# Kernel tuning notes

Measured on AMD Instinct MI355X. Metric: run time of the kernel, lower is better.

The kernel has to match this reference:

```python
import jax, jax.numpy as jnp
from jax import lax
import numpy as np

# Straight-through-estimator sign (standard BNN binarization):
# fwd: sign(x) with sign(0)=+1; bwd: pass gradient where |x|<=1 (hardtanh STE).
@jax.custom_vjp
def sign_ste(x):
    return jnp.where(x >= 0, 1.0, -1.0).astype(x.dtype)

def _sign_fwd(x):
    return sign_ste(x), x

def _sign_bwd(x, g):
    return (g * (jnp.abs(x) <= 1.0).astype(g.dtype),)

sign_ste.defvjp(_sign_fwd, _sign_bwd)

EPS = 1e-5  # BatchNorm eps (torch default)

def bn4(x, g, b):  # BatchNorm2d, training-mode batch stats, x: [N,C,H,W]
    m = x.mean((0, 2, 3), keepdims=True)
    v = x.var((0, 2, 3), keepdims=True)
    return g[None, :, None, None] * (x - m) * lax.rsqrt(v + EPS) + b[None, :, None, None]

def bn1(x, g, b):  # BatchNorm1d, x: [N,C]
    m = x.mean(0, keepdims=True)
    v = x.var(0, keepdims=True)
    return g * (x - m) * lax.rsqrt(v + EPS) + b

def bconv(x, W, b, first):
    # BinarizedConv2d: binarize weights always; binarize input except first layer.
    xb = x if first else sign_ste(x)
    y = lax.conv_general_dilated(xb, sign_ste(W), (1, 1), [(1, 1), (1, 1)],
                                 dimension_numbers=('NCHW', 'OIHW', 'NCHW'))
    return y + b[None, :, None, None]

def maxpool2(x):
    return lax.reduce_window(x, -jnp.inf, lax.max, (1, 1, 2, 2), (1, 1, 2, 2), 'VALID')

def ht(x):  # Hardtanh
    return jnp.clip(x, -1.0, 1.0)

CONV_CH = [(3, 64), (64, 128), (128, 256), (256, 256), (256, 512), (512, 512), (512, 512), (512, 512)]
LIN_CH = [(512, 512), (512, 512), (512, 10)]
POOL_AFTER = (0, 1, 3, 5, 7)  # conv indices followed by MaxPool2d

def setup_inputs():
    key = jax.random.key(0)
    ks = iter(jax.random.split(key, 64))
    d = {"x": jax.random.normal(next(ks), (256, 3, 32, 32), jnp.float32)}
    for i, (ci, co) in enumerate(CONV_CH):
        d[f"cw{i}"] = jax.random.normal(next(ks), (co, ci, 3, 3), jnp.float32) * 0.1
        d[f"cb{i}"] = jnp.zeros((co,), jnp.float32)
        d[f"cg{i}"] = jnp.ones((co,), jnp.float32)
        d[f"ct{i}"] = jnp.zeros((co,), jnp.float32)
    for i, (ci, co) in enumerate(LIN_CH):
        d[f"lw{i}"] = jax.random.normal(next(ks), (co, ci), jnp.float32) * 0.1
        d[f"lb{i}"] = jnp.zeros((co,), jnp.float32)
        d[f"lg{i}"] = jnp.ones((co,), jnp.float32)
        d[f"lt{i}"] = jnp.zeros((co,), jnp.float32)
    return d

def _forward(x, cw, cb, cg, ct, lw, lb, lg, lt):
    h = x
    for i in range(8):
        h = bconv(h, cw[i], cb[i], i == 0)
        if i in POOL_AFTER:
            h = maxpool2(h)
        h = ht(bn4(h, cg[i], ct[i]))
    h = h.reshape(h.shape[0], -1)  # [N, 512] after 5 pools on 32x32
    for i in range(3):
        h = sign_ste(h) @ sign_ste(lw[i]).T + lb[i]  # BinarizedLinear
        h = bn1(h, lg[i], lt[i])
        if i < 2:
            h = ht(h)  # Dropout is identity in eval mode
    return jax.nn.log_softmax(h, axis=-1)

def reference(x,
              cw0, cb0, cg0, ct0, cw1, cb1, cg1, ct1, cw2, cb2, cg2, ct2,
              cw3, cb3, cg3, ct3, cw4, cb4, cg4, ct4, cw5, cb5, cg5, ct5,
              cw6, cb6, cg6, ct6, cw7, cb7, cg7, ct7,
              lw0, lb0, lg0, lt0, lw1, lb1, lg1, lt1, lw2, lb2, lg2, lt2):
    cw = [cw0, cw1, cw2, cw3, cw4, cw5, cw6, cw7]
    cb = [cb0, cb1, cb2, cb3, cb4, cb5, cb6, cb7]
    cg = [cg0, cg1, cg2, cg3, cg4, cg5, cg6, cg7]
    ct = [ct0, ct1, ct2, ct3, ct4, ct5, ct6, ct7]
    lw = [lw0, lw1, lw2]
    lb = [lb0, lb1, lb2]
    lg = [lg0, lg1, lg2]
    lt = [lt0, lt1, lt2]
    return _forward(x, cw, cb, cg, ct, lw, lb, lg, lt)
```

## Files before the change

kernel.cpp:

```cpp
#include <hip/hip_runtime.h>
#include <hip/hip_bf16.h>

typedef unsigned long long u64;

#define EPSV 1e-5

__device__ __forceinline__ int imax(int a, int b) { return a > b ? a : b; }
__device__ __forceinline__ int iclamp(int v, int lo, int hi) { return v < lo ? lo : (v > hi ? hi : v); }

struct PrepArgs {
    const float* src[10];
    u64* dst[10];
    int CW[10];
    int Co[10];
    int taps[10];
    int rowbase[11];
    u64* accs;
    int naccs;
};

__global__ __launch_bounds__(256) void prep_kernel(PrepArgs a) {
    __shared__ float buf[4608];
    const int blk = blockIdx.x;
    int z = blk * 19 + threadIdx.x;
    if (threadIdx.x < 19 && z < a.naccs) a.accs[z] = 0ULL;

    int l = 0;
    while (l < 9 && blk >= a.rowbase[l + 1]) ++l;
    const int row = blk - a.rowbase[l];
    const int CW = a.CW[l];
    const int taps = a.taps[l];
    const int nf = CW * 64 * taps;
    const float* srow = a.src[l] + (size_t)row * nf;
    for (int i = threadIdx.x; i < nf; i += 256) buf[i] = srow[i];
    __syncthreads();
    const int t = threadIdx.x;
    if (t < taps * CW) {
        u64 bits = 0;
        if (taps == 9) {
            int k = t % 9, w = t / 9;
            for (int j = 0; j < 64; ++j) bits |= (u64)(buf[(w * 64 + j) * 9 + k] >= 0.f) << j;
            a.dst[l][(size_t)(k * CW + w) * a.Co[l] + row] = bits;
        } else {
            for (int j = 0; j < 64; ++j) bits |= (u64)(buf[t * 64 + j] >= 0.f) << j;
            a.dst[l][(size_t)row * CW + t] = bits;
        }
    }
}

__global__ __launch_bounds__(256) void conv0_lane(const float* __restrict__ x,
                                                  const float* __restrict__ wgt,
                                                  float* __restrict__ out,
                                                  double* __restrict__ dacc) {
    const int lane = threadIdx.x & 63;
    const int wave = threadIdx.x >> 6;
    float ws[27];
#pragma unroll
    for (int j = 0; j < 27; ++j) ws[j] = (wgt[lane * 27 + j] >= 0.f) ? 1.f : -1.f;

    const int gp0 = blockIdx.x * 32;
    const int n = gp0 >> 8;
    const int ypA = (gp0 >> 4) & 15;
    const int yb = 2 * ypA - 1;

    __shared__ float simg[3][6][34];
    const float* xb = x + (size_t)n * 3072;
    for (int t = threadIdx.x; t < 612; t += 256) {
        int ci = t / 204;
        int rem = t % 204;
        int r = rem / 34;
        int cc = rem % 34;
        int yy = yb + r;
        int xx = cc - 1;
        float v = 0.f;
        if ((unsigned)yy < 32u && (unsigned)xx < 32u) v = xb[(ci * 32 + yy) * 32 + xx];
        simg[ci][r][cc] = v;
    }
    __syncthreads();

    double s1 = 0.0, s2 = 0.0;
#pragma unroll 2
    for (int pi = 0; pi < 8; ++pi) {
        const int lp = wave * 8 + pi;
        const int gp = gp0 + lp;
        const int xp = lp & 15;
        const int rbase = 2 * (lp >> 4);
        const int cbase = 2 * xp;
        float win[3][4][4];
#pragma unroll
        for (int ci = 0; ci < 3; ++ci)
#pragma unroll
            for (int r = 0; r < 4; ++r)
#pragma unroll
                for (int c = 0; c < 4; ++c) win[ci][r][c] = simg[ci][rbase + r][cbase + c];
        float a00 = 0.f, a01 = 0.f, a10 = 0.f, a11 = 0.f;
#pragma unroll
        for (int ci = 0; ci < 3; ++ci)
#pragma unroll
            for (int ky = 0; ky < 3; ++ky)
#pragma unroll
                for (int kx = 0; kx < 3; ++kx) {
                    float wv = ws[ci * 9 + ky * 3 + kx];
                    a00 += win[ci][ky][kx] * wv;
                    a01 += win[ci][ky][kx + 1] * wv;
                    a10 += win[ci][ky + 1][kx] * wv;
                    a11 += win[ci][ky + 1][kx + 1] * wv;
                }
        float val = fmaxf(fmaxf(a00, a01), fmaxf(a10, a11));
        out[(size_t)gp * 64 + lane] = val;
        s1 += (double)val;
        s2 += (double)val * (double)val;
    }
    __shared__ double sh1[4][64], sh2[4][64];
    sh1[wave][lane] = s1;
    sh2[wave][lane] = s2;
    __syncthreads();
    if (threadIdx.x < 64) {
        double t1 = 0.0, t2 = 0.0;
#pragma unroll
        for (int r = 0; r < 4; ++r) { t1 += sh1[r][threadIdx.x]; t2 += sh2[r][threadIdx.x]; }
        double* sh = dacc + (size_t)(blockIdx.x & 7) * 1024;
        atomicAdd(&sh[2 * threadIdx.x], t1);
        atomicAdd(&sh[2 * threadIdx.x + 1], t2);
    }
}

__global__ __launch_bounds__(256) void bnpack_i(const short* __restrict__ in,
                                                const u64* __restrict__ iacc,
                                                const float* __restrict__ g,
                                                const float* __restrict__ b,
                                                u64* __restrict__ act, int Co, int wshift,
                                                int count) {
    __shared__ int2 sthr[520];
    for (int i = threadIdx.x; i < Co; i += 256) {
        long long S1 = 0, S2 = 0;
#pragma unroll
        for (int s = 0; s < 8; ++s) {
            S1 += (long long)iacc[s * 1024 + 2 * i];
            S2 += (long long)iacc[s * 1024 + 2 * i + 1];
        }
        double m = (double)S1 / count;
        double var = (double)S2 / count - m * m;
        double sc = (double)g[i] / sqrt(var + EPSV);
        int2 r;
        if (sc == 0.0) r = make_int2(b[i] >= 0.f ? (int)0x80000000 : 0x7fffffff, 0);
        else {
            double t = m - (double)b[i] / sc;
            if (t > 1.0e9) t = 1.0e9;
            if (t < -1.0e9) t = -1.0e9;
            r = (sc > 0.0) ? make_int2((int)ceil(t), 0) : make_int2((int)floor(t), 1);
        }
        sthr[(i >> 6) * 65 + (i & 63)] = r;
    }
    __syncthreads();
    int tid = blockIdx.x * 256 + threadIdx.x;
    int part = tid & 3;
    int word = tid >> 2;
    int w = word & ((1 << wshift) - 1);
    int pix = word >> wshift;
    const int4* r4 = (const int4*)(in + (size_t)pix * Co + (w << 6) + part * 16);
    u64 bits = 0;
#pragma unroll
    for (int q = 0; q < 2; ++q) {
        int4 v = r4[q];
        int words4[4] = {v.x, v.y, v.z, v.w};
#pragma unroll
        for (int u = 0; u < 4; ++u) {
#pragma unroll
            for (int h = 0; h < 2; ++h) {
                int c = part * 16 + q * 8 + u * 2 + h;
                int val = (int)(short)((h == 0) ? (words4[u] & 0xffff) : ((unsigned)words4[u] >> 16));
                int2 t = sthr[w * 65 + c];
                bool bit = t.y ? (val <= t.x) : (val >= t.x);
                bits |= (u64)bit << c;
            }
        }
    }
    bits |= __shfl_xor(bits, 1);
    bits |= __shfl_xor(bits, 2);
    if (part == 0) act[word] = bits;
}

template <int CW, int HIN, bool POOL, int WC, bool INTERIOR>
__device__ __forceinline__ void row_accum(const u64* __restrict__ inb,
                                          const u64* __restrict__ wpkT, int Co, int co,
                                          const int* yoff, const bool* ry, int* cnt) {
    constexpr int HP = POOL ? HIN / 2 : HIN;
    constexpr int WS = POOL ? 4 : 3;
    constexpr int NA = POOL ? 4 : 1;
#pragma unroll 1
    for (int w0 = 0; w0 < CW; w0 += WC) {
        u64 wg[9 * WC];
#pragma unroll
        for (int k = 0; k < 9; ++k)
#pragma unroll
            for (int w = 0; w < WC; ++w)
                wg[k * WC + w] = wpkT[(size_t)(k * CW + w0 + w) * Co + co];
        u64 cur[WS][WS][WC];
#pragma unroll
        for (int d = 0; d < WS; ++d) {
            int cc = d - 1;
            int ccc = cc < 0 ? 0 : cc;
#pragma unroll
            for (int r = 0; r < WS; ++r) {
                const u64* p = inb + yoff[r] + ccc * CW + w0;
                if (WC == 1) {
                    cur[r][d][0] = p[0];
                } else {
                    ulonglong2 v = *(const ulonglong2*)p;
                    cur[r][d][0] = v.x;
                    cur[r][d][1] = v.y;
                }
            }
        }
#pragma unroll
        for (int xp = 0; xp < HP; ++xp) {
            if constexpr (POOL) {
#pragma unroll
                for (int py = 0; py < 2; ++py)
#pragma unroll
                    for (int qx = 0; qx < 2; ++qx)
#pragma unroll
                        for (int ky = 0; ky < 3; ++ky)
#pragma unroll
                            for (int kx = 0; kx < 3; ++kx) {
                                int d = qx + kx;
                                int cc = 2 * xp + d - 1;
                                if (cc >= 0 && cc < HIN) {
#pragma unroll
                                    for (int w = 0; w < WC; ++w) {
                                        int pc = (int)__popcll(cur[py + ky][d][w] ^
                                                               wg[(ky * 3 + kx) * WC + w]);
                                        if constexpr (INTERIOR)
                                            cnt[xp * NA + py * 2 + qx] += pc;
                                        else
                                            cnt[xp * NA + py * 2 + qx] += ry[py + ky] ? pc : 0;
                                    }
                                }
                            }
            } else {
#pragma unroll
                for (int ky = 0; ky < 3; ++ky)
#pragma unroll
                    for (int kx = 0; kx < 3; ++kx) {
                        int cc = xp + kx - 1;
                        if (cc >= 0 && cc < HIN) {
#pragma unroll
                            for (int w = 0; w < WC; ++w) {
                                int pc = (int)__popcll(cur[ky][kx][w] ^
                                                       wg[(ky * 3 + kx) * WC + w]);
                                if constexpr (INTERIOR)
                                    cnt[xp] += pc;
                                else
                                    cnt[xp] += ry[ky] ? pc : 0;
                            }
                        }
                    }
            }
            if (xp < HP - 1) {
                if constexpr (POOL) {
#pragma unroll
                    for (int r = 0; r < WS; ++r)
#pragma unroll
                        for (int w = 0; w < WC; ++w) {
                            cur[r][0][w] = cur[r][2][w];
                            cur[r][1][w] = cur[r][3][w];
                        }
#pragma unroll
                    for (int dd = 2; dd < 4; ++dd) {
                        int cc = 2 * (xp + 1) + dd - 1;
                        int ccc = cc >= HIN ? HIN - 1 : cc;
#pragma unroll
                        for (int r = 0; r < WS; ++r) {
                            const u64* p = inb + yoff[r] + ccc * CW + w0;
                            if (WC == 1) {
                                cur[r][dd][0] = p[0];
                            } else {
                                ulonglong2 v = *(const ulonglong2*)p;
                                cur[r][dd][0] = v.x;
                                cur[r][dd][1] = v.y;
                            }
                        }
                    }
                } else {
#pragma unroll
                    for (int r = 0; r < WS; ++r)
#pragma unroll
                        for (int w = 0; w < WC; ++w) {
                            cur[r][0][w] = cur[r][1][w];
                            cur[r][1][w] = cur[r][2][w];
                        }
                    int cc = xp + 2;
                    int ccc = cc >= HIN ? HIN - 1 : cc;
#pragma unroll
                    for (int r = 0; r < WS; ++r) {
                        const u64* p = inb + yoff[r] + ccc * CW + w0;
                        if (WC == 1) {
                            cur[r][2][0] = p[0];
                        } else {
                            ulonglong2 v = *(const ulonglong2*)p;
                            cur[r][2][0] = v.x;
                            cur[r][2][1] = v.y;
                        }
                    }
                }
            }
        }
    }
}

template <int CW, int HIN, bool POOL, int WC, bool FIRST>
__global__ __launch_bounds__(256) void bconv_row_f(const void* __restrict__ inprev,
                                                   const void* __restrict__ pstats,
                                                   const float* __restrict__ pg,
                                                   const float* __restrict__ pb, int pcount,
                                                   const u64* __restrict__ wpkT,
                                                   short* __restrict__ out,
                                                   u64* __restrict__ iacc, int Co) {
    constexpr int HP = POOL ? HIN / 2 : HIN;
    constexpr int WS = POOL ? 4 : 3;
    constexpr int NA = POOL ? 4 : 1;
    constexpr int ROWS = POOL ? 10 : 6;
    constexpr int Ci = CW * 64;
    __shared__ __align__(16) u64 sU[ROWS * HIN * CW];
    __shared__ int2 sthr[CW * 65];
    __shared__ float2 sthf[64];

    if constexpr (FIRST) {
        if (threadIdx.x < 64) {
            const double* dacc = (const double*)pstats;
            int i = threadIdx.x;
            double S1 = 0.0, S2 = 0.0;
#pragma unroll
            for (int s = 0; s < 8; ++s) {
                S1 += dacc[s * 1024 + 2 * i];
                S2 += dacc[s * 1024 + 2 * i + 1];
            }
            double m = S1 / pcount;
            double var = S2 / pcount - m * m;
            double sc = (double)pg[i] / sqrt(var + EPSV);
            float2 r;
            if (sc == 0.0) r = make_float2(pb[i] >= 0.f ? -3.0e38f : 3.0e38f, 1.f);
            else {
                double t = m - (double)pb[i] / sc;
                r = make_float2((float)t, sc > 0.0 ? 1.f : -1.f);
            }
            sthf[i] = r;
        }
    } else {
        const u64* pacc = (const u64*)pstats;
        for (int i = threadIdx.x; i < Ci; i += 256) {
            long long S1 = 0, S2 = 0;
#pragma unroll
            for (int s = 0; s < 8; ++s) {
                S1 += (long long)pacc[s * 1024 + 2 * i];
                S2 += (long long)pacc[s * 1024 + 2 * i + 1];
            }
            double m = (double)S1 / pcount;
            double var = (double)S2 / pcount - m * m;
            double sc = (double)pg[i] / sqrt(var + EPSV);
            int2 r;
            if (sc == 0.0) r = make_int2(pb[i] >= 0.f ? (int)0x80000000 : 0x7fffffff, 0);
            else {
                double t = m - (double)pb[i] / sc;
                if (t > 1.0e9) t = 1.0e9;
                if (t < -1.0e9) t = -1.0e9;
                r = (sc > 0.0) ? make_int2((int)ceil(t), 0) : make_int2((int)floor(t), 1);
            }
            sthr[(i >> 6) * 65 + (i & 63)] = r;
        }
    }
    __syncthreads();

    const int bi = blockIdx.x;
    constexpr int BPN = HP / 4;
    const int n = bi / BPN;
    const int yp0 = (bi % BPN) * 4;
    const int ylo = imax(0, (POOL ? 2 * yp0 : yp0) - 1);
    const int yhiU = POOL ? (2 * yp0 + 8) : (yp0 + 4);
    const int yhi = yhiU > HIN - 1 ? HIN - 1 : yhiU;
    const int nrows = yhi - ylo + 1;
    const int nw = nrows * HIN * CW;

    if constexpr (FIRST) {
        const float* src = (const float*)inprev;
        for (int t = threadIdx.x; t < nw; t += 256) {
            int x = t % HIN;
            int yr = t / HIN;
            int y = ylo + yr;
            const float4* p = (const float4*)(src + (size_t)((n * 16 + y) * 16 + x) * 64);
            u64 bits = 0;
#pragma unroll
            for (int q = 0; q < 16; ++q) {
                float4 v = p[q];
                float vv[4] = {v.x, v.y, v.z, v.w};
#pragma unroll
                for (int u = 0; u < 4; ++u) {
                    int c = q * 4 + u;
                    float2 th = sthf[c];
                    bool bit = (th.y > 0.f) ? (vv[u] >= th.x) : (vv[u] <= th.x);
                    bits |= (u64)bit << c;
                }
            }
            sU[t] = bits;
        }
    } else {
        const short* src = (const short*)inprev;
        for (int t = threadIdx.x; t < nw; t += 256) {
            int w = t % CW;
            int x = (t / CW) % HIN;
            int yr = t / (HIN * CW);
            int y = ylo + yr;
            const int4* p = (const int4*)(src + (size_t)((n * HIN + y) * HIN + x) * Ci + w * 64);
            u64 bits = 0;
#pragma unroll
            for (int q = 0; q < 8; ++q) {
                int4 v = p[q];
                int wd[4] = {v.x, v.y, v.z, v.w};
#pragma unroll
                for (int u = 0; u < 4; ++u) {
#pragma unroll
                    for (int h = 0; h < 2; ++h) {
                        int j = q * 8 + u * 2 + h;
                        int val = (int)(short)((h == 0) ? (wd[u] & 0xffff) : ((unsigned)wd[u] >> 16));
                        int2 th = sthr[w * 65 + j];
                        bool bit = th.y ? (val <= th.x) : (val >= th.x);
                        bits |= (u64)bit << j;
                    }
                }
            }
            sU[t] = bits;
        }
    }
    __syncthreads();

    const int lane = threadIdx.x & 63;
    const int wave = threadIdx.x >> 6;
    const int co = blockIdx.y * 64 + lane;
    const int yp = yp0 + wave;
    const int grow = n * HP + yp;
    const int y0 = (POOL ? 2 * yp : yp) - 1;
    int yoff[WS];
    bool ry[WS];
#pragma unroll
    for (int r = 0; r < WS; ++r) {
        int y = y0 + r;
        ry[r] = (unsigned)y < (unsigned)HIN;
        int yc = iclamp(y, 0, HIN - 1);
        yoff[r] = (yc - ylo) * (HIN * CW);
    }
    int cnt[HP * NA];
#pragma unroll
    for (int i = 0; i < HP * NA; ++i) cnt[i] = 0;

    if (yp > 0 && yp < HP - 1)
        row_accum<CW, HIN, POOL, WC, true>(sU, wpkT, Co, co, yoff, ry, cnt);
    else
        row_accum<CW, HIN, POOL, WC, false>(sU, wpkT, Co, co, yoff, ry, cnt);

    const int nr0 = (int)ry[0] + (int)ry[1] + (int)ry[2];
    const int nr1 = POOL ? ((int)ry[1] + (int)ry[2] + (int)ry[WS - 1]) : 0;

    int s1 = 0;
    long long s2 = 0;
    short* orow = out + (size_t)grow * HP * Co + co;
#pragma unroll
    for (int xp = 0; xp < HP; ++xp) {
        int ival;
        if constexpr (POOL) {
            int best = -2147483647;
#pragma unroll
            for (int py = 0; py < 2; ++py) {
                const int nrv = py ? nr1 : nr0;
#pragma unroll
                for (int qx = 0; qx < 2; ++qx) {
                    int ncols = 3;
                    if (xp == 0 && qx == 0) ncols = 2;
                    if (xp == HP - 1 && qx == 1) ncols = 2;
                    int v = 64 * CW * nrv * ncols - 2 * cnt[xp * NA + py * 2 + qx];
                    best = imax(best, v);
                }
            }
            ival = best;
        } else {
            const int ncols = (xp == 0 || xp == HIN - 1) ? 2 : 3;
            ival = 64 * CW * nr0 * ncols - 2 * cnt[xp];
        }
        orow[(size_t)xp * Co] = (short)ival;
        s1 += ival;
        s2 += (long long)ival * ival;
    }

    __shared__ u64 sacc[128];
    if (threadIdx.x < 128) sacc[threadIdx.x] = 0ULL;
    __syncthreads();
    atomicAdd(&sacc[lane], (u64)(long long)s1);
    atomicAdd(&sacc[64 + lane], (u64)s2);
    __syncthreads();
    u64* sh = iacc + (size_t)(blockIdx.x & 7) * 1024;
    if (threadIdx.x < 64)
        atomicAdd(&sh[2 * (blockIdx.y * 64 + threadIdx.x)], sacc[threadIdx.x]);
    else if (threadIdx.x < 128)
        atomicAdd(&sh[2 * (blockIdx.y * 64 + threadIdx.x - 64) + 1], sacc[threadIdx.x]);
}

template <int CW, int HIN, bool POOL>
__global__ __launch_bounds__(256) void bconv_tiny_f(const short* __restrict__ inprev,
                                                    const u64* __restrict__ pacc,
                                                    const float* __restrict__ pg,
                                                    const float* __restrict__ pb, int pcount,
                                                    const u64* __restrict__ wpkT,
                                                    short* __restrict__ out,
                                                    u64* __restrict__ iacc, int Co) {
    constexpr int NPX = HIN * HIN;
    constexpr int HP = POOL ? HIN / 2 : HIN;
    constexpr int Ci = CW * 64;
    __shared__ int2 sthr[CW * 65];
    __shared__ u64 sU[4][NPX * CW];

    for (int i = threadIdx.x; i < Ci; i += 256) {
        long long S1 = 0, S2 = 0;
#pragma unroll
        for (int s = 0; s < 8; ++s) {
            S1 += (long long)pacc[s * 1024 + 2 * i];
            S2 += (long long)pacc[s * 1024 + 2 * i + 1];
        }
        double m = (double)S1 / pcount;
        double var = (double)S2 / pcount - m * m;
        double sc = (double)pg[i] / sqrt(var + EPSV);
        int2 r;
        if (sc == 0.0) r = make_int2(pb[i] >= 0.f ? (int)0x80000000 : 0x7fffffff, 0);
        else {
            double t = m - (double)pb[i] / sc;
            if (t > 1.0e9) t = 1.0e9;
            if (t < -1.0e9) t = -1.0e9;
            r = (sc > 0.0) ? make_int2((int)ceil(t), 0) : make_int2((int)floor(t), 1);
        }
        sthr[(i >> 6) * 65 + (i & 63)] = r;
    }
    __syncthreads();

    const int nbase = blockIdx.x * 4;
    for (int t = threadIdx.x; t < 4 * NPX * CW; t += 256) {
        int img = t / (NPX * CW);
        int rem = t % (NPX * CW);
        int w = rem % CW;
        int i = rem / CW;
        const int4* p = (const int4*)(inprev + (size_t)((nbase + img) * NPX + i) * Ci + w * 64);
        u64 bits = 0;
#pragma unroll
        for (int q = 0; q < 8; ++q) {
            int4 v = p[q];
            int wd[4] = {v.x, v.y, v.z, v.w};
#pragma unroll
            for (int u = 0; u < 4; ++u) {
#pragma unroll
                for (int h = 0; h < 2; ++h) {
                    int j = q * 8 + u * 2 + h;
                    int val = (int)(short)((h == 0) ? (wd[u] & 0xffff) : ((unsigned)wd[u] >> 16));
                    int2 th = sthr[w * 65 + j];
                    bool bit = th.y ? (val <= th.x) : (val >= th.x);
                    bits |= (u64)bit << j;
                }
            }
        }
        sU[img][i * CW + w] = bits;
    }
    __syncthreads();

    const int lane = threadIdx.x & 63;
    const int co = blockIdx.y * 64 + lane;
    const int n = nbase + (threadIdx.x >> 6);
    const u64* inb = sU[threadIdx.x >> 6];
    int cnt[NPX];
#pragma unroll
    for (int i = 0; i < NPX; ++i) cnt[i] = 0;

#pragma unroll 2
    for (int w = 0; w < CW; ++w) {
        u64 win[NPX];
#pragma unroll
        for (int i = 0; i < NPX; ++i) win[i] = inb[i * CW + w];
#pragma unroll
        for (int k = 0; k < 9; ++k) {
            u64 wb = wpkT[(size_t)(k * CW + w) * Co + co];
            const int ky = k / 3, kx = k % 3;
#pragma unroll
            for (int py = 0; py < HIN; ++py)
#pragma unroll
                for (int px = 0; px < HIN; ++px) {
                    const int yy = py + ky - 1, xx = px + kx - 1;
                    if (yy >= 0 && yy < HIN && xx >= 0 && xx < HIN)
                        cnt[py * HIN + px] += (int)__popcll(win[yy * HIN + xx] ^ wb);
                }
        }
    }

    int fin[NPX];
#pragma unroll
    for (int py = 0; py < HIN; ++py)
#pragma unroll
        for (int px = 0; px < HIN; ++px) {
            const int nk = ((py == 0 || py == HIN - 1) ? 2 : 3) *
                           ((px == 0 || px == HIN - 1) ? 2 : 3);
            fin[py * HIN + px] = 64 * CW * nk - 2 * cnt[py * HIN + px];
        }

    short vals[HP * HP];
    if constexpr (POOL) {
#pragma unroll
        for (int py = 0; py < HP; ++py)
#pragma unroll
            for (int px = 0; px < HP; ++px)
                vals[py * HP + px] = (short)imax(
                    imax(fin[(2 * py) * HIN + 2 * px], fin[(2 * py) * HIN + 2 * px + 1]),
                    imax(fin[(2 * py + 1) * HIN + 2 * px], fin[(2 * py + 1) * HIN + 2 * px + 1]));
    } else {
#pragma unroll
        for (int i = 0; i < NPX; ++i) vals[i] = (short)fin[i];
    }
#pragma unroll
    for (int p = 0; p < HP * HP; ++p) out[(size_t)(n * HP * HP + p) * Co + co] = vals[p];

    long long s1 = 0, s2 = 0;
#pragma unroll
    for (int p = 0; p < HP * HP; ++p) {
        s1 += vals[p];
        s2 += (long long)vals[p] * vals[p];
    }
    __shared__ u64 sacc[128];
    if (threadIdx.x < 128) sacc[threadIdx.x] = 0ULL;
    __syncthreads();
    atomicAdd(&sacc[lane], (u64)s1);
    atomicAdd(&sacc[64 + lane], (u64)s2);
    __syncthreads();
    u64* sh = iacc + (size_t)(blockIdx.x & 7) * 1024;
    if (threadIdx.x < 64)
        atomicAdd(&sh[2 * (blockIdx.y * 64 + threadIdx.x)], sacc[threadIdx.x]);
    else if (threadIdx.x < 128)
        atomicAdd(&sh[2 * (blockIdx.y * 64 + threadIdx.x - 64) + 1], sacc[threadIdx.x]);
}

__global__ __launch_bounds__(256) void lin_kernel(const u64* __restrict__ hp,
                                                  const u64* __restrict__ wp,
                                                  const float* __restrict__ lb,
                                                  const float* __restrict__ g,
                                                  const float* __restrict__ bta,
                                                  u64* __restrict__ op) {
    int o = blockIdx.x;
    int n = threadIdx.x;
    const u64* hr = hp + n * 8;
    const u64* wr = wp + o * 8;
    int s = 0;
#pragma unroll
    for (int w = 0; w < 8; ++w) s += (int)__popcll(hr[w] ^ wr[w]);
    float val = (float)(512 - 2 * s) + lb[o];
    __shared__ double sh1[256], sh2[256];
    sh1[n] = (double)val;
    sh2[n] = (double)val * (double)val;
    __syncthreads();
    for (int st = 128; st > 0; st >>= 1) {
        if (n < st) {
            sh1[n] += sh1[n + st];
            sh2[n] += sh2[n + st];
        }
        __syncthreads();
    }
    __shared__ float sm, siv;
    if (n == 0) {
        double m = sh1[0] / 256.0;
        double var = sh2[0] / 256.0 - m * m;
        sm = (float)m;
        siv = (float)(1.0 / sqrt(var + EPSV));
    }
    __syncthreads();
    float zz = g[o] * (val - sm) * siv + bta[o];
    if (zz >= 0.f) atomicOr(&op[(size_t)n * 8 + (o >> 6)], 1ULL << (o & 63));
}

__global__ __launch_bounds__(256) void lin2_lsm(const u64* __restrict__ hp,
                                                const u64* __restrict__ wp,
                                                const float* __restrict__ lb,
                                                const float* __restrict__ g,
                                                const float* __restrict__ bta,
                                                float* __restrict__ out) {
    const int n = threadIdx.x;
    const int lane = n & 63;
    const int wave = n >> 6;
    u64 h[8];
#pragma unroll
    for (int w = 0; w < 8; ++w) h[w] = hp[n * 8 + w];
    float v[10];
#pragma unroll
    for (int o = 0; o < 10; ++o) {
        int s = 0;
#pragma unroll
        for (int w = 0; w < 8; ++w) s += (int)__popcll(h[w] ^ wp[o * 8 + w]);
        v[o] = (float)(512 - 2 * s) + lb[o];
    }
    __shared__ double w1[4][10], w2[4][10];
#pragma unroll
    for (int o = 0; o < 10; ++o) {
        double a = (double)v[o];
        double b = a * a;
#pragma unroll
        for (int off = 32; off > 0; off >>= 1) {
            a += __shfl_xor(a, off);
            b += __shfl_xor(b, off);
        }
        if (lane == 0) {
            w1[wave][o] = a;
            w2[wave][o] = b;
        }
    }
    __syncthreads();
    float z[10];
#pragma unroll
    for (int o = 0; o < 10; ++o) {
        double S1 = w1[0][o] + w1[1][o] + w1[2][o] + w1[3][o];
        double S2 = w2[0][o] + w2[1][o] + w2[2][o] + w2[3][o];
        double m = S1 / 256.0;
        double var = S2 / 256.0 - m * m;
        float sm = (float)m;
        float siv = (float)(1.0 / sqrt(var + EPSV));
        z[o] = g[o] * (v[o] - sm) * siv + bta[o];
    }
    float mx = z[0];
#pragma unroll
    for (int o = 1; o < 10; ++o) mx = fmaxf(mx, z[o]);
    float se = 0.f;
#pragma unroll
    for (int o = 0; o < 10; ++o) se += expf(z[o] - mx);
    float ls = logf(se);
#pragma unroll
    for (int o = 0; o < 10; ++o) out[n * 10 + o] = z[o] - mx - ls;
}

extern "C" void kernel_launch(void* const* d_in, const int* in_sizes, int n_in, void* d_out,
                              int out_size, void* d_ws, size_t ws_size, hipStream_t stream) {
    (void)in_sizes; (void)n_in; (void)out_size; (void)ws_size;
    const float* x = (const float*)d_in[0];
    const float *cw[8], *cb[8], *cg[8], *ct[8];
    for (int i = 0; i < 8; ++i) {
        cw[i] = (const float*)d_in[1 + 4 * i];
        cb[i] = (const float*)d_in[2 + 4 * i];
        cg[i] = (const float*)d_in[3 + 4 * i];
        ct[i] = (const float*)d_in[4 + 4 * i];
    }
    const float *lw[3], *lb[3], *lg[3], *lt[3];
    for (int i = 0; i < 3; ++i) {
        lw[i] = (const float*)d_in[33 + 4 * i];
        lb[i] = (const float*)d_in[34 + 4 * i];
        lg[i] = (const float*)d_in[35 + 4 * i];
        lt[i] = (const float*)d_in[36 + 4 * i];
    }

    static const int CIs[8] = {3, 64, 128, 256, 256, 512, 512, 512};
    static const int COs[8] = {64, 128, 256, 256, 512, 512, 512, 512};

    char* ws = (char*)d_ws;
    size_t off = 0;
    auto alloc = [&](size_t bytes) -> void* {
        void* p = ws + off;
        off += (bytes + 255) & ~(size_t)255;
        return p;
    };

    u64* accs = (u64*)alloc((size_t)8 * 8 * 1024 * 8);
    u64* fcs0 = (u64*)alloc(2048 * 8);
    u64* fcs1 = (u64*)alloc(2048 * 8);
    double* dacc0 = (double*)accs;
    auto iacc = [&](int layer) { return accs + (size_t)layer * 8192; };

    u64* wpkT[8] = {};
    for (int i = 1; i < 8; ++i) wpkT[i] = (u64*)alloc((size_t)COs[i] * 9 * (CIs[i] / 64) * 8);
    u64* wpl[3];
    int LO[3] = {512, 512, 10};
    for (int i = 0; i < 3; ++i) wpl[i] = (u64*)alloc((size_t)LO[i] * 8 * 8);
    u64* act7 = (u64*)alloc((size_t)256 * 8 * 8);
    float* out0 = (float*)alloc((size_t)65536 * 64 * 4);
    short* i16A = (short*)alloc((size_t)16384 * 256 * 2);
    short* i16B = (short*)alloc((size_t)16384 * 256 * 2);

    PrepArgs pa;
    int rb = 0;
    for (int i = 1; i < 8; ++i) {
        int e = i - 1;
        pa.src[e] = cw[i];
        pa.dst[e] = wpkT[i];
        pa.CW[e] = CIs[i] / 64;
        pa.Co[e] = COs[i];
        pa.taps[e] = 9;
        pa.rowbase[e] = rb;
        rb += COs[i];
    }
    for (int i = 0; i < 3; ++i) {
        int e = 7 + i;
        pa.src[e] = lw[i];
        pa.dst[e] = wpl[i];
        pa.CW[e] = 8;
        pa.Co[e] = LO[i];
        pa.taps[e] = 1;
        pa.rowbase[e] = rb;
        rb += LO[i];
    }
    pa.rowbase[10] = rb;
    pa.accs = accs;
    pa.naccs = 8 * 8 * 1024 + 2048 + 2048;
    prep_kernel<<<rb, 256, 0, stream>>>(pa);

    conv0_lane<<<2048, 256, 0, stream>>>(x, cw[0], out0, dacc0);

    bconv_row_f<1, 16, true, 1, true><<<dim3(512, 2), 256, 0, stream>>>(
        out0, dacc0, cg[0], ct[0], 65536, wpkT[1], i16A, iacc(1), 128);

    bconv_row_f<2, 8, false, 2, false><<<dim3(512, 4), 256, 0, stream>>>(
        i16A, iacc(1), cg[1], ct[1], 16384, wpkT[2], i16B, iacc(2), 256);

    bconv_row_f<4, 8, true, 2, false><<<dim3(256, 4), 256, 0, stream>>>(
        i16B, iacc(2), cg[2], ct[2], 16384, wpkT[3], i16A, iacc(3), 256);

    bconv_row_f<4, 4, false, 2, false><<<dim3(256, 8), 256, 0, stream>>>(
        i16A, iacc(3), cg[3], ct[3], 4096, wpkT[4], i16B, iacc(4), 512);

    bconv_tiny_f<8, 4, true><<<dim3(64, 8), 256, 0, stream>>>(
        i16B, iacc(4), cg[4], ct[4], 4096, wpkT[5], i16A, iacc(5), 512);

    bconv_tiny_f<8, 2, false><<<dim3(64, 8), 256, 0, stream>>>(
        i16A, iacc(5), cg[5], ct[5], 1024, wpkT[6], i16B, iacc(6), 512);

    bconv_tiny_f<8, 2, true><<<dim3(64, 8), 256, 0, stream>>>(
        i16B, iacc(6), cg[6], ct[6], 1024, wpkT[7], i16A, iacc(7), 512);

    bnpack_i<<<32, 256, 0, stream>>>(i16A, iacc(7), cg[7], ct[7], act7, 512, 3, 256);

    lin_kernel<<<512, 256, 0, stream>>>(act7, wpl[0], lb[0], lg[0], lt[0], fcs0);
    lin_kernel<<<512, 256, 0, stream>>>(fcs0, wpl[1], lb[1], lg[1], lt[1], fcs1);
    lin2_lsm<<<1, 256, 0, stream>>>(fcs1, wpl[2], lb[2], lg[2], lt[2], (float*)d_out);
}
```

Baseline: 405.9 us.

## Merge weight prep into conv0 launch and restructure linear head kernels

Weight binarization blocks are folded into the conv0 kernel as extra blocks sharing one launch, and the accumulator zeroing moves to a memset. The linear layers now write float outputs that separate pack kernels turn into bits, replacing the atomicOr packing and the single-block final layer with separate linear and log-softmax kernels. Vector 128-bit loads in the conv inner loop become scalar loads, and BN threshold code is factored into a helper. The net launch count goes up in the head, and the scalar loads may cost memory throughput.

```diff
diff --git a/kernel.cpp b/kernel.cpp
--- a/kernel.cpp
+++ b/kernel.cpp
@@ -7,6 +7,21 @@
 
 __device__ __forceinline__ int imax(int a, int b) { return a > b ? a : b; }
 __device__ __forceinline__ int iclamp(int v, int lo, int hi) { return v < lo ? lo : (v > hi ? hi : v); }
+
+__device__ __forceinline__ int2 thr_int(long long S1, long long S2, float gv, float bv, int count) {
+    double m = (double)S1 / count;
+    double var = (double)S2 / count - m * m;
+    double sc = (double)gv / sqrt(var + EPSV);
+    int2 r;
+    if (sc == 0.0) r = make_int2(bv >= 0.f ? (int)0x80000000 : 0x7fffffff, 0);
+    else {
+        double t = m - (double)bv / sc;
+        if (t > 1.0e9) t = 1.0e9;
+        if (t < -1.0e9) t = -1.0e9;
+        r = (sc > 0.0) ? make_int2((int)ceil(t), 0) : make_int2((int)floor(t), 1);
+    }
+    return r;
+}
 
 struct PrepArgs {
     const float* src[10];
@@ -15,43 +30,40 @@
     int Co[10];
     int taps[10];
     int rowbase[11];
-    u64* accs;
-    int naccs;
 };
 
-__global__ __launch_bounds__(256) void prep_kernel(PrepArgs a) {
-    __shared__ float buf[4608];
-    const int blk = blockIdx.x;
-    int z = blk * 19 + threadIdx.x;
-    if (threadIdx.x < 19 && z < a.naccs) a.accs[z] = 0ULL;
-
-    int l = 0;
-    while (l < 9 && blk >= a.rowbase[l + 1]) ++l;
-    const int row = blk - a.rowbase[l];
-    const int CW = a.CW[l];
-    const int taps = a.taps[l];
-    const int nf = CW * 64 * taps;
-    const float* srow = a.src[l] + (size_t)row * nf;
-    for (int i = threadIdx.x; i < nf; i += 256) buf[i] = srow[i];
-    __syncthreads();
-    const int t = threadIdx.x;
-    if (t < taps * CW) {
-        u64 bits = 0;
-        if (taps == 9) {
-            int k = t % 9, w = t / 9;
-            for (int j = 0; j < 64; ++j) bits |= (u64)(buf[(w * 64 + j) * 9 + k] >= 0.f) << j;
-            a.dst[l][(size_t)(k * CW + w) * a.Co[l] + row] = bits;
-        } else {
-            for (int j = 0; j < 64; ++j) bits |= (u64)(buf[t * 64 + j] >= 0.f) << j;
-            a.dst[l][(size_t)row * CW + t] = bits;
-        }
-    }
-}
-
-__global__ __launch_bounds__(256) void conv0_lane(const float* __restrict__ x,
+__global__ __launch_bounds__(256) void prep_conv0(PrepArgs a, const float* __restrict__ x,
                                                   const float* __restrict__ wgt,
                                                   float* __restrict__ out,
                                                   double* __restrict__ dacc) {
+    __shared__ __align__(16) char smem[18432];
+    if (blockIdx.x >= 2048) {
+        float* buf = (float*)smem;
+        const int blk = blockIdx.x - 2048;
+        int l = 0;
+        while (l < 9 && blk >= a.rowbase[l + 1]) ++l;
+        const int row = blk - a.rowbase[l];
+        const int CW = a.CW[l];
+        const int taps = a.taps[l];
+        const int nf = CW * 64 * taps;
+        const float* srow = a.src[l] + (size_t)row * nf;
+        for (int i = threadIdx.x; i < nf; i += 256) buf[i] = srow[i];
+        __syncthreads();
+        const int t = threadIdx.x;
+        if (t < taps * CW) {
+            u64 bits = 0;
+            if (taps == 9) {
+                int k = t % 9, w = t / 9;
+                for (int j = 0; j < 64; ++j) bits |= (u64)(buf[(w * 64 + j) * 9 + k] >= 0.f) << j;
+                a.dst[l][(size_t)(k * CW + w) * a.Co[l] + row] = bits;
+            } else {
+                for (int j = 0; j < 64; ++j) bits |= (u64)(buf[t * 64 + j] >= 0.f) << j;
+                a.dst[l][(size_t)row * CW + t] = bits;
+            }
+        }
+        return;
+    }
+
     const int lane = threadIdx.x & 63;
     const int wave = threadIdx.x >> 6;
     float ws[27];
@@ -63,7 +75,10 @@
     const int ypA = (gp0 >> 4) & 15;
     const int yb = 2 * ypA - 1;
 
-    __shared__ float simg[3][6][34];
+    float* simg = (float*)smem;
+    double* sh1 = (double*)(smem + 4096);
+    double* sh2 = (double*)(smem + 6144);
+
     const float* xb = x + (size_t)n * 3072;
     for (int t = threadIdx.x; t < 612; t += 256) {
         int ci = t / 204;
@@ -74,7 +89,7 @@
         int xx = cc - 1;
         float v = 0.f;
         if ((unsigned)yy < 32u && (unsigned)xx < 32u) v = xb[(ci * 32 + yy) * 32 + xx];
-        simg[ci][r][cc] = v;
+        simg[(ci * 6 + r) * 34 + cc] = v;
     }
     __syncthreads();
 
@@ -92,7 +107,7 @@
 #pragma unroll
             for (int r = 0; r < 4; ++r)
 #pragma unroll
-                for (int c = 0; c < 4; ++c) win[ci][r][c] = simg[ci][rbase + r][cbase + c];
+                for (int c = 0; c < 4; ++c) win[ci][r][c] = simg[(ci * 6 + rbase + r) * 34 + cbase + c];
         float a00 = 0.f, a01 = 0.f, a10 = 0.f, a11 = 0.f;
 #pragma unroll
         for (int ci = 0; ci < 3; ++ci)
@@ -111,14 +126,16 @@
         s1 += (double)val;
         s2 += (double)val * (double)val;
     }
-    __shared__ double sh1[4][64], sh2[4][64];
-    sh1[wave][lane] = s1;
-    sh2[wave][lane] = s2;
+    sh1[wave * 64 + lane] = s1;
+    sh2[wave * 64 + lane] = s2;
     __syncthreads();
     if (threadIdx.x < 64) {
         double t1 = 0.0, t2 = 0.0;
 #pragma unroll
-        for (int r = 0; r < 4; ++r) { t1 += sh1[r][threadIdx.x]; t2 += sh2[r][threadIdx.x]; }
+        for (int r = 0; r < 4; ++r) {
+            t1 += sh1[r * 64 + threadIdx.x];
+            t2 += sh2[r * 64 + threadIdx.x];
+        }
         double* sh = dacc + (size_t)(blockIdx.x & 7) * 1024;
         atomicAdd(&sh[2 * threadIdx.x], t1);
         atomicAdd(&sh[2 * threadIdx.x + 1], t2);
@@ -139,18 +156,7 @@
             S1 += (long long)iacc[s * 1024 + 2 * i];
             S2 += (long long)iacc[s * 1024 + 2 * i + 1];
         }
-        double m = (double)S1 / count;
-        double var = (double)S2 / count - m * m;
-        double sc = (double)g[i] / sqrt(var + EPSV);
-        int2 r;
-        if (sc == 0.0) r = make_int2(b[i] >= 0.f ? (int)0x80000000 : 0x7fffffff, 0);
-        else {
-            double t = m - (double)b[i] / sc;
-            if (t > 1.0e9) t = 1.0e9;
-            if (t < -1.0e9) t = -1.0e9;
-            r = (sc > 0.0) ? make_int2((int)ceil(t), 0) : make_int2((int)floor(t), 1);
-        }
-        sthr[(i >> 6) * 65 + (i & 63)] = r;
+        sthr[(i >> 6) * 65 + (i & 63)] = thr_int(S1, S2, g[i], b[i], count);
     }
     __syncthreads();
     int tid = blockIdx.x * 256 + threadIdx.x;
@@ -207,9 +213,8 @@
                 if (WC == 1) {
                     cur[r][d][0] = p[0];
                 } else {
-                    ulonglong2 v = *(const ulonglong2*)p;
-                    cur[r][d][0] = v.x;
-                    cur[r][d][1] = v.y;
+                    cur[r][d][0] = p[0];
+                    cur[r][d][1] = p[1];
                 }
             }
         }
@@ -276,9 +281,8 @@
                             if (WC == 1) {
                                 cur[r][dd][0] = p[0];
                             } else {
-                                ulonglong2 v = *(const ulonglong2*)p;
-                                cur[r][dd][0] = v.x;
-                                cur[r][dd][1] = v.y;
+                                cur[r][dd][0] = p[0];
+                                cur[r][dd][1] = p[1];
                             }
                         }
                     }
@@ -298,9 +302,8 @@
                         if (WC == 1) {
                             cur[r][2][0] = p[0];
                         } else {
-                            ulonglong2 v = *(const ulonglong2*)p;
-                            cur[r][2][0] = v.x;
-                            cur[r][2][1] = v.y;
+                            cur[r][2][0] = p[0];
+                            cur[r][2][1] = p[1];
                         }
                     }
                 }
@@ -356,18 +359,7 @@
                 S1 += (long long)pacc[s * 1024 + 2 * i];
                 S2 += (long long)pacc[s * 1024 + 2 * i + 1];
             }
-            double m = (double)S1 / pcount;
-            double var = (double)S2 / pcount - m * m;
-            double sc = (double)pg[i] / sqrt(var + EPSV);
-            int2 r;
-            if (sc == 0.0) r = make_int2(pb[i] >= 0.f ? (int)0x80000000 : 0x7fffffff, 0);
-            else {
-                double t = m - (double)pb[i] / sc;
-                if (t > 1.0e9) t = 1.0e9;
-                if (t < -1.0e9) t = -1.0e9;
-                r = (sc > 0.0) ? make_int2((int)ceil(t), 0) : make_int2((int)floor(t), 1);
-            }
-            sthr[(i >> 6) * 65 + (i & 63)] = r;
+            sthr[(i >> 6) * 65 + (i & 63)] = thr_int(S1, S2, pg[i], pb[i], pcount);
         }
     }
     __syncthreads();
@@ -525,18 +517,7 @@
             S1 += (long long)pacc[s * 1024 + 2 * i];
             S2 += (long long)pacc[s * 1024 + 2 * i + 1];
         }
-        double m = (double)S1 / pcount;
-        double var = (double)S2 / pcount - m * m;
-        double sc = (double)pg[i] / sqrt(var + EPSV);
-        int2 r;
-        if (sc == 0.0) r = make_int2(pb[i] >= 0.f ? (int)0x80000000 : 0x7fffffff, 0);
-        else {
-            double t = m - (double)pb[i] / sc;
-            if (t > 1.0e9) t = 1.0e9;
-            if (t < -1.0e9) t = -1.0e9;
-            r = (sc > 0.0) ? make_int2((int)ceil(t), 0) : make_int2((int)floor(t), 1);
-        }
-        sthr[(i >> 6) * 65 + (i & 63)] = r;
+        sthr[(i >> 6) * 65 + (i & 63)] = thr_int(S1, S2, pg[i], pb[i], pcount);
     }
     __syncthreads();
 
@@ -646,7 +627,7 @@
                                                   const float* __restrict__ lb,
                                                   const float* __restrict__ g,
                                                   const float* __restrict__ bta,
-                                                  u64* __restrict__ op) {
+                                                  float* __restrict__ z, int O, int applyHt) {
     int o = blockIdx.x;
     int n = threadIdx.x;
     const u64* hr = hp + n * 8;
@@ -675,75 +656,55 @@
     }
     __syncthreads();
     float zz = g[o] * (val - sm) * siv + bta[o];
-    if (zz >= 0.f) atomicOr(&op[(size_t)n * 8 + (o >> 6)], 1ULL << (o & 63));
-}
-
-__global__ __launch_bounds__(256) void lin2_lsm(const u64* __restrict__ hp,
-                                                const u64* __restrict__ wp,
-                                                const float* __restrict__ lb,
-                                                const float* __restrict__ g,
-                                                const float* __restrict__ bta,
-                                                float* __restrict__ out) {
-    const int n = threadIdx.x;
-    const int lane = n & 63;
-    const int wave = n >> 6;
-    u64 h[8];
-#pragma unroll
-    for (int w = 0; w < 8; ++w) h[w] = hp[n * 8 + w];
+    if (applyHt) zz = fminf(1.f, fmaxf(-1.f, zz));
+    z[(size_t)n * O + o] = zz;
+}
+
+__global__ void pack_rows(const float* __restrict__ z, u64* __restrict__ hp) {
+    int tid = blockIdx.x * 256 + threadIdx.x;
+    int part = tid & 3;
+    int word = tid >> 2;
+    int ww = word & 7;
+    int n = word >> 3;
+    const float4* r4 = (const float4*)(z + (size_t)n * 512 + (ww << 6) + part * 16);
+    u64 bits = 0;
+#pragma unroll
+    for (int q = 0; q < 4; ++q) {
+        float4 v = r4[q];
+        float vv[4] = {v.x, v.y, v.z, v.w};
+#pragma unroll
+        for (int u = 0; u < 4; ++u) bits |= (u64)(vv[u] >= 0.f) << (part * 16 + q * 4 + u);
+    }
+    bits |= __shfl_xor(bits, 1);
+    bits |= __shfl_xor(bits, 2);
+    if (part == 0) hp[word] = bits;
+}
+
+__global__ void lsm_kernel(const float* __restrict__ z, float* __restrict__ out) {
+    int n = blockIdx.x * 64 + threadIdx.x;
+    if (n >= 256) return;
     float v[10];
-#pragma unroll
-    for (int o = 0; o < 10; ++o) {
-        int s = 0;
-#pragma unroll
-        for (int w = 0; w < 8; ++w) s += (int)__popcll(h[w] ^ wp[o * 8 + w]);
-        v[o] = (float)(512 - 2 * s) + lb[o];
-    }
-    __shared__ double w1[4][10], w2[4][10];
-#pragma unroll
-    for (int o = 0; o < 10; ++o) {
-        double a = (double)v[o];
-        double b = a * a;
-#pragma unroll
-        for (int off = 32; off > 0; off >>= 1) {
-            a += __shfl_xor(a, off);
-            b += __shfl_xor(b, off);
-        }
-        if (lane == 0) {
-            w1[wave][o] = a;
-            w2[wave][o] = b;
-        }
-    }
-    __syncthreads();
-    float z[10];
-#pragma unroll
-    for (int o = 0; o < 10; ++o) {
-        double S1 = w1[0][o] + w1[1][o] + w1[2][o] + w1[3][o];
-        double S2 = w2[0][o] + w2[1][o] + w2[2][o] + w2[3][o];
-        double m = S1 / 256.0;
-        double var = S2 / 256.0 - m * m;
-        float sm = (float)m;
-        float siv = (float)(1.0 / sqrt(var + EPSV));
-        z[o] = g[o] * (v[o] - sm) * siv + bta[o];
-    }
-    float mx = z[0];
-#pragma unroll
-    for (int o = 1; o < 10; ++o) mx = fmaxf(mx, z[o]);
-    float se = 0.f;
-#pragma unroll
-    for (int o = 0; o < 10; ++o) se += expf(z[o] - mx);
-    float ls = logf(se);
-#pragma unroll
-    for (int o = 0; o < 10; ++o) out[n * 10 + o] = z[o] - mx - ls;
+    float m = -1e30f;
+#pragma unroll
+    for (int i = 0; i < 10; ++i) {
+        v[i] = z[n * 10 + i];
+        m = fmaxf(m, v[i]);
+    }
+    float s = 0.f;
+#pragma unroll
+    for (int i = 0; i < 10; ++i) s += expf(v[i] - m);
+    float ls = logf(s);
+#pragma unroll
+    for (int i = 0; i < 10; ++i) out[n * 10 + i] = v[i] - m - ls;
 }
 
 extern "C" void kernel_launch(void* const* d_in, const int* in_sizes, int n_in, void* d_out,
                               int out_size, void* d_ws, size_t ws_size, hipStream_t stream) {
     (void)in_sizes; (void)n_in; (void)out_size; (void)ws_size;
     const float* x = (const float*)d_in[0];
-    const float *cw[8], *cb[8], *cg[8], *ct[8];
+    const float *cw[8], *cg[8], *ct[8];
     for (int i = 0; i < 8; ++i) {
         cw[i] = (const float*)d_in[1 + 4 * i];
-        cb[i] = (const float*)d_in[2 + 4 * i];
         cg[i] = (const float*)d_in[3 + 4 * i];
         ct[i] = (const float*)d_in[4 + 4 * i];
     }
@@ -767,8 +728,6 @@
     };
 
     u64* accs = (u64*)alloc((size_t)8 * 8 * 1024 * 8);
-    u64* fcs0 = (u64*)alloc(2048 * 8);
-    u64* fcs1 = (u64*)alloc(2048 * 8);
     double* dacc0 = (double*)accs;
     auto iacc = [&](int layer) { return accs + (size_t)layer * 8192; };
 
@@ -778,9 +737,16 @@
     int LO[3] = {512, 512, 10};
     for (int i = 0; i < 3; ++i) wpl[i] = (u64*)alloc((size_t)LO[i] * 8 * 8);
     u64* act7 = (u64*)alloc((size_t)256 * 8 * 8);
+    u64* fcs0 = (u64*)alloc(2048 * 8);
+    u64* fcs1 = (u64*)alloc(2048 * 8);
     float* out0 = (float*)alloc((size_t)65536 * 64 * 4);
     short* i16A = (short*)alloc((size_t)16384 * 256 * 2);
     short* i16B = (short*)alloc((size_t)16384 * 256 * 2);
+    float* z0 = (float*)alloc((size_t)256 * 512 * 4);
+    float* z1 = (float*)alloc((size_t)256 * 512 * 4);
+    float* z2 = (float*)alloc((size_t)256 * 10 * 4);
+
+    hipMemsetAsync(accs, 0, (size_t)8 * 8 * 1024 * 8, stream);
 
     PrepArgs pa;
     int rb = 0;
@@ -805,11 +771,7 @@
         rb += LO[i];
     }
     pa.rowbase[10] = rb;
-    pa.accs = accs;
-    pa.naccs = 8 * 8 * 1024 + 2048 + 2048;
-    prep_kernel<<<rb, 256, 0, stream>>>(pa);
-
-    conv0_lane<<<2048, 256, 0, stream>>>(x, cw[0], out0, dacc0);
+    prep_conv0<<<2048 + rb, 256, 0, stream>>>(pa, x, cw[0], out0, dacc0);
 
     bconv_row_f<1, 16, true, 1, true><<<dim3(512, 2), 256, 0, stream>>>(
         out0, dacc0, cg[0], ct[0], 65536, wpkT[1], i16A, iacc(1), 128);
@@ -834,7 +796,10 @@
 
     bnpack_i<<<32, 256, 0, stream>>>(i16A, iacc(7), cg[7], ct[7], act7, 512, 3, 256);
 
-    lin_kernel<<<512, 256, 0, stream>>>(act7, wpl[0], lb[0], lg[0], lt[0], fcs0);
-    lin_kernel<<<512, 256, 0, stream>>>(fcs0, wpl[1], lb[1], lg[1], lt[1], fcs1);
-    lin2_lsm<<<1, 256, 0, stream>>>(fcs1, wpl[2], lb[2], lg[2], lt[2], (float*)d_out);
-}
+    lin_kernel<<<512, 256, 0, stream>>>(act7, wpl[0], lb[0], lg[0], lt[0], z0, 512, 1);
+    pack_rows<<<32, 256, 0, stream>>>(z0, fcs0);
+    lin_kernel<<<512, 256, 0, stream>>>(fcs0, wpl[1], lb[1], lg[1], lt[1], z1, 512, 1);
+    pack_rows<<<32, 256, 0, stream>>>(z1, fcs1);
+    lin_kernel<<<10, 256, 0, stream>>>(fcs1, wpl[2], lb[2], lg[2], lt[2], z2, 10, 0);
+    lsm_kernel<<<4, 64, 0, stream>>>(z2, (float*)d_out);
+}
```

Result: no change. 398.0 us (-1.9%).
